# Kernel optimization log

Measured on AMD Instinct MI355X. Metric: run time of the kernel, lower is better.

Reference implementation:

```python
import jax, jax.numpy as jnp
import numpy as np

N_NODE = 2048   # n_node
N_TIME = 10     # t / look_back
STEP_K = 5
PROB_C = 0.98
LN_EPS = 1e-5


def setup_inputs() -> dict:
    key = jax.random.key(0)
    k1, k2 = jax.random.split(key, 2)
    # dynamic adjacency-like input: [n_node, n_time, n_node], nonnegative
    x = jax.random.uniform(k1, (N_NODE, N_TIME, N_NODE), dtype=jnp.float32)
    # learned restart weights, init = prob_c (already in [0,1])
    weight = jnp.full((N_TIME, STEP_K), PROB_C, dtype=jnp.float32)
    # LayerNorm(n_node) params
    ln_gamma = jnp.ones((N_NODE,), dtype=jnp.float32)
    ln_beta = jnp.zeros((N_NODE,), dtype=jnp.float32)
    return {"x": x, "weight": weight, "ln_gamma": ln_gamma, "ln_beta": ln_beta}


def _layer_norm(h, gamma, beta):
    mu = jnp.mean(h, axis=-1, keepdims=True)
    var = jnp.mean((h - mu) ** 2, axis=-1, keepdims=True)
    return (h - mu) * jax.lax.rsqrt(var + LN_EPS) * gamma + beta


def reference(x, weight, ln_gamma, ln_beta):
    # x: [N, T, N]; weight: [T, K]
    w = jnp.clip(weight, 0.0, 1.0)
    n = x.shape[0]
    eye = jnp.eye(n, dtype=x.dtype)  # Pt0

    G = jnp.transpose(x, (1, 0, 2))                 # [T, N, N]
    deg = jnp.sum(G, axis=-1, keepdims=True) + 1e-8  # row degree
    G_norm = G / deg                                # D^{-1} G (row-normalize)

    def per_time(Gt_norm, wt):
        # random walk with restart, accumulate sum of P over K steps
        def step(carry, wi):
            P, acc = carry
            Pc = wi * (P @ Gt_norm) + (1.0 - wi) * eye
            return (Pc, acc + Pc), None
        (_, final_P), _ = jax.lax.scan(step, (eye, jnp.zeros_like(eye)), wt)
        return _layer_norm(final_P, ln_gamma, ln_beta)

    out = jax.vmap(per_time)(G_norm, w)  # [T, N, N]
    return jnp.transpose(out, (1, 0, 2))  # [N, T, N]
```

## Files before the change

kernel.cpp:

```cpp
#include <hip/hip_runtime.h>
#include <stdint.h>

#define NN 2048
#define TT 10
#define KST 5
#define BK 64
#define NKT2 (NN / BK)

typedef float f32x4 __attribute__((ext_vector_type(4)));
typedef __bf16 bf16x8 __attribute__((ext_vector_type(8)));
typedef unsigned short u16x8 __attribute__((ext_vector_type(8)));

using as3_void = __attribute__((address_space(3))) void;
using as1_const_void = const __attribute__((address_space(1))) void;

__device__ __forceinline__ unsigned short f2bf_bits(float f) {
    unsigned u = __builtin_bit_cast(unsigned, f);
    unsigned r = u + 0x7FFFu + ((u >> 16) & 1u);
    return (unsigned short)(r >> 16);
}
__device__ __forceinline__ float bf2f(unsigned short b) {
    return __builtin_bit_cast(float, ((unsigned)b) << 16);
}

__global__ __launch_bounds__(256) void deg_kernel(const float* __restrict__ x,
                                                  float* __restrict__ deg) {
    const int i = blockIdx.x;
    const int t = blockIdx.y;
    const int tid = threadIdx.x;
    const float4* r4 = (const float4*)(x + ((size_t)i * TT + t) * NN);
    float4 a = r4[tid];
    float4 b = r4[tid + 256];
    float s = a.x + a.y + a.z + a.w + b.x + b.y + b.z + b.w;
    #pragma unroll
    for (int m = 32; m >= 1; m >>= 1) s += __shfl_xor(s, m, 64);
    __shared__ float red[4];
    if ((tid & 63) == 0) red[tid >> 6] = s;
    __syncthreads();
    if (tid == 0) deg[(size_t)t * NN + i] = red[0] + red[1] + red[2] + red[3] + 1e-8f;
}

__global__ __launch_bounds__(256) void gnt_init_kernel(const float* __restrict__ x,
                                                       const float* __restrict__ deg,
                                                       const float* __restrict__ w,
                                                       unsigned short* __restrict__ gnt,
                                                       unsigned short* __restrict__ p1,
                                                       int t0) {
    const int tl = blockIdx.z;
    const int t  = t0 + tl;
    float w0 = w[t * KST + 0];
    w0 = fminf(fmaxf(w0, 0.0f), 1.0f);
    const float om = 1.0f - w0;
    const int n0 = blockIdx.x * 64;
    const int k0 = blockIdx.y * 64;
    __shared__ float tile[64][65];
    const int tx = threadIdx.x & 63;
    const int ty = threadIdx.x >> 6;
    unsigned short* p1dst = p1 + (size_t)tl * NN * NN;
    #pragma unroll
    for (int p = 0; p < 16; ++p) {
        int kr = p * 4 + ty;
        float rd = 1.0f / deg[(size_t)t * NN + k0 + kr];
        float v = x[(((size_t)(k0 + kr)) * TT + t) * NN + n0 + tx] * rd;
        tile[kr][tx] = v;
        float pv = w0 * v + ((k0 + kr) == (n0 + tx) ? om : 0.0f);
        p1dst[(size_t)(k0 + kr) * NN + n0 + tx] = f2bf_bits(pv);
    }
    __syncthreads();
    unsigned short* dst = gnt + (size_t)tl * NN * NN;
    #pragma unroll
    for (int p = 0; p < 16; ++p) {
        int nr = p * 4 + ty;
        dst[(size_t)(n0 + nr) * NN + k0 + tx] = f2bf_bits(tile[tx][nr]);
    }
}

#define FENCE __asm__ volatile("" ::: "memory")
#define LGKM0 do { __asm__ volatile("s_waitcnt lgkmcnt(0)" ::: "memory"); \
                   __builtin_amdgcn_sched_barrier(0); } while (0)

#define MFMA_PHASE(PA, PB, BARR)                                                  \
  do {                                                                            \
    _Pragma("unroll")                                                             \
    for (int f_ = 0; f_ < 4; ++f_) {                                              \
      _Pragma("unroll")                                                           \
      for (int g_ = 0; g_ < 2; ++g_) {                                            \
        acc[(PA)*4 + f_][(PB)*2 + g_] = __builtin_amdgcn_mfma_f32_16x16x32_bf16(  \
            af[f_][0], BARR[g_][0], acc[(PA)*4 + f_][(PB)*2 + g_], 0, 0, 0);      \
        acc[(PA)*4 + f_][(PB)*2 + g_] = __builtin_amdgcn_mfma_f32_16x16x32_bf16(  \
            af[f_][1], BARR[g_][1], acc[(PA)*4 + f_][(PB)*2 + g_], 0, 0, 0);      \
      }                                                                           \
    }                                                                             \
  } while (0)

__global__ __launch_bounds__(512, 2) void gemm_step256(
        const unsigned short* __restrict__ Pprev,
        const unsigned short* __restrict__ gnt,
        const float* __restrict__ w,
        unsigned short* __restrict__ Pnext,
        int t0, int kstep) {
    extern __shared__ char smem[];

    const int nwg  = (int)gridDim.x;
    const int flat = (int)blockIdx.x;
    const int xcd  = flat & 7;
    const int q    = nwg >> 3, r = nwg & 7;
    const int wgid = (xcd < r ? xcd * (q + 1) : r * (q + 1) + (xcd - r) * q) + (flat >> 3);
    const int tl   = wgid >> 6;
    const int s    = wgid & 63;
    const int g4   = s >> 2, w4 = s & 3;
    const int tm   = ((g4 >> 2) << 1) | (w4 >> 1);
    const int tn   = ((g4 & 3) << 1) | (w4 & 1);
    const int t    = t0 + tl;

    const int tid  = threadIdx.x;
    const int lane = tid & 63;
    const int wv   = tid >> 6;
    const int wm   = wv >> 2;
    const int wn   = wv & 3;
    const int lr   = lane & 15;
    const int quad = lane >> 4;
    const int swz  = lr & 7;

    const unsigned short* Ab = Pprev + (size_t)tl * NN * NN;
    const unsigned short* Bb = gnt   + (size_t)tl * NN * NN;

    const int srow  = lane >> 3;
    const int sslot = (lane & 7) ^ srow;
    const unsigned short* pa[2][2];
    const unsigned short* pb[2][2];
    #pragma unroll
    for (int h = 0; h < 2; ++h)
        #pragma unroll
        for (int l = 0; l < 2; ++l) {
            const int rA = tm * 256 + h * 128 + l * 64 + wv * 8 + srow;
            const int rB = tn * 256 + h * 128 + l * 64 + wv * 8 + srow;
            pa[h][l] = Ab + (size_t)rA * NN + sslot * 8;
            pb[h][l] = Bb + (size_t)rB * NN + sslot * 8;
        }

    auto stageA = [&](int kt, int b, int h) {
        #pragma unroll
        for (int l = 0; l < 2; ++l)
            __builtin_amdgcn_global_load_lds(
                (as1_const_void*)(pa[h][l] + kt * BK),
                (as3_void*)(smem + b * 65536 + h * 16384 + l * 8192 + wv * 1024),
                16, 0, 0);
    };
    auto stageB = [&](int kt, int b, int h) {
        #pragma unroll
        for (int l = 0; l < 2; ++l)
            __builtin_amdgcn_global_load_lds(
                (as1_const_void*)(pb[h][l] + kt * BK),
                (as3_void*)(smem + b * 65536 + 32768 + h * 16384 + l * 8192 + wv * 1024),
                16, 0, 0);
    };

    bf16x8 af[4][2];
    bf16x8 bf0[2][2];
    bf16x8 bf1[2][2];
    const int sA = ((quad)     ^ swz) * 16;
    const int sB = ((quad + 4) ^ swz) * 16;
    auto lda = [&](int b, int half) {
        const char* base = smem + b * 65536 + half * 16384 + (wm * 64 + lr) * 128;
        #pragma unroll
        for (int f = 0; f < 4; ++f) {
            af[f][0] = *(const bf16x8*)(base + f * 2048 + sA);
            af[f][1] = *(const bf16x8*)(base + f * 2048 + sB);
        }
    };
    auto ldb = [&](int b, int half, bf16x8 (&dst)[2][2]) {
        const char* base = smem + b * 65536 + 32768 + half * 16384 + (wn * 32 + lr) * 128;
        #pragma unroll
        for (int g = 0; g < 2; ++g) {
            dst[g][0] = *(const bf16x8*)(base + g * 2048 + sA);
            dst[g][1] = *(const bf16x8*)(base + g * 2048 + sB);
        }
    };

    f32x4 acc[8][4];
    #pragma unroll
    for (int i = 0; i < 8; ++i)
        #pragma unroll
        for (int j = 0; j < 4; ++j)
            acc[i][j] = (f32x4){0.0f, 0.0f, 0.0f, 0.0f};

    stageA(0, 0, 0);
    stageB(0, 0, 0);
    stageB(0, 0, 1);
    stageA(0, 0, 1);
    stageA(1, 1, 0);
    stageB(1, 1, 0);
    stageB(1, 1, 1);
    FENCE; __builtin_amdgcn_s_waitcnt(0xF76); __builtin_amdgcn_s_barrier(); FENCE;

    for (int kt = 0; kt < NKT2; ++kt) {
        const int b  = kt & 1;
        const int nb = b ^ 1;
        const int k1 = (kt + 1 < NKT2) ? kt + 1 : NKT2 - 1;
        const int k2 = (kt + 2 < NKT2) ? kt + 2 : NKT2 - 1;

        lda(b, 0);
        ldb(b, 0, bf0);
        stageA(k1, nb, 1);
        FENCE; __builtin_amdgcn_s_barrier(); LGKM0;
        __builtin_amdgcn_s_setprio(1);
        MFMA_PHASE(0, 0, bf0);
        __builtin_amdgcn_s_setprio(0);
        FENCE; __builtin_amdgcn_s_barrier(); FENCE;

        ldb(b, 1, bf1);
        stageA(k2, b, 0);
        FENCE; __builtin_amdgcn_s_barrier(); LGKM0;
        __builtin_amdgcn_s_setprio(1);
        MFMA_PHASE(0, 1, bf1);
        __builtin_amdgcn_s_setprio(0);
        FENCE; __builtin_amdgcn_s_barrier(); FENCE;

        lda(b, 1);
        stageB(k2, b, 0);
        FENCE; __builtin_amdgcn_s_barrier(); LGKM0;
        __builtin_amdgcn_s_setprio(1);
        MFMA_PHASE(1, 1, bf1);
        __builtin_amdgcn_s_setprio(0);
        FENCE; __builtin_amdgcn_s_barrier(); FENCE;

        stageB(k2, b, 1);
        __builtin_amdgcn_s_setprio(1);
        MFMA_PHASE(1, 0, bf0);
        __builtin_amdgcn_s_setprio(0);
        FENCE; __builtin_amdgcn_s_waitcnt(0xF76); __builtin_amdgcn_s_barrier(); FENCE;
    }

    float wk = w[t * KST + kstep];
    wk = fminf(fmaxf(wk, 0.0f), 1.0f);
    const float om = 1.0f - wk;
    unsigned short* __restrict__ Pn = Pnext + (size_t)tl * NN * NN;
    #pragma unroll
    for (int F = 0; F < 8; ++F) {
        const int mrow0 = tm * 256 + (F >> 2) * 128 + wm * 64 + (F & 3) * 16 + quad * 4;
        #pragma unroll
        for (int v = 0; v < 4; ++v) {
            const int m = mrow0 + v;
            const size_t mb = (size_t)m * NN;
            #pragma unroll
            for (int G = 0; G < 4; ++G) {
                const int n = tn * 256 + (G >> 1) * 128 + wn * 32 + (G & 1) * 16 + lr;
                float val = wk * acc[F][G][v] + (m == n ? om : 0.0f);
                Pn[mb + n] = f2bf_bits(val);
            }
        }
    }
}

__global__ __launch_bounds__(256) void ln_kernel(const unsigned short* __restrict__ Pall,
                                                 const float* __restrict__ gamma,
                                                 const float* __restrict__ beta,
                                                 float* __restrict__ out,
                                                 int t0, size_t strideK) {
    const int m  = blockIdx.x;
    const int tl = blockIdx.y;
    const int t  = t0 + tl;
    const int tid = threadIdx.x;
    const int j = tid * 8;

    const size_t rbase = (size_t)tl * NN * NN + (size_t)m * NN + j;
    float v[8] = {0, 0, 0, 0, 0, 0, 0, 0};
    #pragma unroll
    for (int k = 0; k < KST; ++k) {
        u16x8 pv = *(const u16x8*)(Pall + (size_t)k * strideK + rbase);
        #pragma unroll
        for (int e = 0; e < 8; ++e) v[e] += bf2f(pv[e]);
    }

    float s = 0.0f;
    #pragma unroll
    for (int e = 0; e < 8; ++e) s += v[e];
    #pragma unroll
    for (int mm = 32; mm >= 1; mm >>= 1) s += __shfl_xor(s, mm, 64);
    __shared__ float red[4];
    if ((tid & 63) == 0) red[tid >> 6] = s;
    __syncthreads();
    const float mu = (red[0] + red[1] + red[2] + red[3]) * (1.0f / NN);

    float q = 0.0f;
    float dx[8];
    #pragma unroll
    for (int e = 0; e < 8; ++e) { dx[e] = v[e] - mu; q += dx[e] * dx[e]; }
    __syncthreads();
    #pragma unroll
    for (int mm = 32; mm >= 1; mm >>= 1) q += __shfl_xor(q, mm, 64);
    if ((tid & 63) == 0) red[tid >> 6] = q;
    __syncthreads();
    const float var = (red[0] + red[1] + red[2] + red[3]) * (1.0f / NN);
    const float sc = rsqrtf(var + 1e-5f);

    float4 g0 = *(const float4*)(gamma + j);
    float4 g1 = *(const float4*)(gamma + j + 4);
    float4 b0 = *(const float4*)(beta + j);
    float4 b1 = *(const float4*)(beta + j + 4);
    const size_t ob = ((size_t)m * TT + t) * NN + j;
    float4 o0, o1;
    o0.x = dx[0] * sc * g0.x + b0.x;  o0.y = dx[1] * sc * g0.y + b0.y;
    o0.z = dx[2] * sc * g0.z + b0.z;  o0.w = dx[3] * sc * g0.w + b0.w;
    o1.x = dx[4] * sc * g1.x + b1.x;  o1.y = dx[5] * sc * g1.y + b1.y;
    o1.z = dx[6] * sc * g1.z + b1.z;  o1.w = dx[7] * sc * g1.w + b1.w;
    *(float4*)(out + ob)     = o0;
    *(float4*)(out + ob + 4) = o1;
}

extern "C" void kernel_launch(void* const* d_in, const int* in_sizes, int n_in,
                              void* d_out, int out_size, void* d_ws, size_t ws_size,
                              hipStream_t stream) {
    (void)in_sizes; (void)n_in; (void)out_size;
    const float* x     = (const float*)d_in[0];
    const float* w     = (const float*)d_in[1];
    const float* gamma = (const float*)d_in[2];
    const float* beta  = (const float*)d_in[3];
    float* out = (float*)d_out;

    static bool attr_done = false;
    if (!attr_done) {
        (void)hipFuncSetAttribute((const void*)gemm_step256,
                                  hipFuncAttributeMaxDynamicSharedMemorySize, 131072);
        attr_done = true;
    }

    char* ws = (char*)d_ws;
    float* deg = (float*)ws;
    size_t off = ((size_t)TT * NN * sizeof(float) + 255) & ~(size_t)255;
    const size_t per_t = (size_t)NN * NN * sizeof(unsigned short);
    size_t avail = ws_size > off ? ws_size - off : 0;
    int TB = (int)(avail / ((1 + KST) * per_t));
    if (TB < 1) TB = 1;
    if (TB > TT) TB = TT;
    unsigned short* gnt  = (unsigned short*)(ws + off);
    unsigned short* Pall = gnt + (size_t)TB * NN * NN;
    const size_t strideK = (size_t)TB * NN * NN;

    deg_kernel<<<dim3(NN, TT), 256, 0, stream>>>(x, deg);

    for (int t0 = 0; t0 < TT; t0 += TB) {
        const int tb = (TT - t0) < TB ? (TT - t0) : TB;
        gnt_init_kernel<<<dim3(32, 32, tb), 256, 0, stream>>>(x, deg, w, gnt, Pall, t0);
        for (int k = 2; k <= KST; ++k) {
            const unsigned short* Pp = Pall + (size_t)(k - 2) * strideK;
            unsigned short*       Pn = Pall + (size_t)(k - 1) * strideK;
            gemm_step256<<<dim3(64 * tb), 512, 131072, stream>>>(Pp, gnt, w, Pn, t0, k - 1);
        }
        ln_kernel<<<dim3(NN, tb), 256, 0, stream>>>(Pall, gamma, beta, out, t0, strideK);
    }
}
```

Before: 1.091 ms.

## Shrink GEMM tile to 128x256 and simplify to a two-phase prefetch pipeline

The GEMM step kernel's workgroup tile goes from 256x256 to 128x256. That halves the A staging, the accumulators and the LDS footprint (96KB instead of 128KB) and doubles the grid to 128 workgroups per time slice, aiming for better load balance and less tail effect. The main loop changes from four MFMA phases with a two-tile-ahead prefetch to two phases with a one-tile-ahead prefetch, synchronised by vmcnt waits and barriers. The cost is lower arithmetic intensity per tile, more global and L2 traffic for the B operand, and a shallower pipeline that may expose memory latency.

```diff
diff --git a/kernel.cpp b/kernel.cpp
--- a/kernel.cpp
+++ b/kernel.cpp
@@ -76,24 +76,22 @@
 }
 
 #define FENCE __asm__ volatile("" ::: "memory")
-#define LGKM0 do { __asm__ volatile("s_waitcnt lgkmcnt(0)" ::: "memory"); \
-                   __builtin_amdgcn_sched_barrier(0); } while (0)
 
 #define MFMA_PHASE(PA, PB, BARR)                                                  \
   do {                                                                            \
     _Pragma("unroll")                                                             \
-    for (int f_ = 0; f_ < 4; ++f_) {                                              \
+    for (int f_ = 0; f_ < 2; ++f_) {                                              \
       _Pragma("unroll")                                                           \
       for (int g_ = 0; g_ < 2; ++g_) {                                            \
-        acc[(PA)*4 + f_][(PB)*2 + g_] = __builtin_amdgcn_mfma_f32_16x16x32_bf16(  \
-            af[f_][0], BARR[g_][0], acc[(PA)*4 + f_][(PB)*2 + g_], 0, 0, 0);      \
-        acc[(PA)*4 + f_][(PB)*2 + g_] = __builtin_amdgcn_mfma_f32_16x16x32_bf16(  \
-            af[f_][1], BARR[g_][1], acc[(PA)*4 + f_][(PB)*2 + g_], 0, 0, 0);      \
+        acc[(PA)*2 + f_][(PB)*2 + g_] = __builtin_amdgcn_mfma_f32_16x16x32_bf16(  \
+            af[f_][0], BARR[g_][0], acc[(PA)*2 + f_][(PB)*2 + g_], 0, 0, 0);      \
+        acc[(PA)*2 + f_][(PB)*2 + g_] = __builtin_amdgcn_mfma_f32_16x16x32_bf16(  \
+            af[f_][1], BARR[g_][1], acc[(PA)*2 + f_][(PB)*2 + g_], 0, 0, 0);      \
       }                                                                           \
     }                                                                             \
   } while (0)
 
-__global__ __launch_bounds__(512, 2) void gemm_step256(
+__global__ __launch_bounds__(512, 2) void gemm_step128(
         const unsigned short* __restrict__ Pprev,
         const unsigned short* __restrict__ gnt,
         const float* __restrict__ w,
@@ -106,12 +104,13 @@
     const int xcd  = flat & 7;
     const int q    = nwg >> 3, r = nwg & 7;
     const int wgid = (xcd < r ? xcd * (q + 1) : r * (q + 1) + (xcd - r) * q) + (flat >> 3);
-    const int tl   = wgid >> 6;
-    const int s    = wgid & 63;
-    const int g4   = s >> 2, w4 = s & 3;
-    const int tm   = ((g4 >> 2) << 1) | (w4 >> 1);
-    const int tn   = ((g4 & 3) << 1) | (w4 & 1);
-    const int t    = t0 + tl;
+    const int tl   = wgid >> 7;
+    const int s    = wgid & 127;
+    const int within = s & 3;
+    const int sup    = s >> 2;
+    const int tm     = (sup >> 2) * 2 + (within >> 1);
+    const int tn     = (sup & 3) * 2 + (within & 1);
+    const int t      = t0 + tl;
 
     const int tid  = threadIdx.x;
     const int lane = tid & 63;
@@ -127,50 +126,49 @@
 
     const int srow  = lane >> 3;
     const int sslot = (lane & 7) ^ srow;
-    const unsigned short* pa[2][2];
+    const unsigned short* pa[2];
     const unsigned short* pb[2][2];
     #pragma unroll
-    for (int h = 0; h < 2; ++h)
+    for (int h = 0; h < 2; ++h) {
+        const int rA = tm * 128 + h * 64 + wv * 8 + srow;
+        pa[h] = Ab + (size_t)rA * NN + sslot * 8;
         #pragma unroll
         for (int l = 0; l < 2; ++l) {
-            const int rA = tm * 256 + h * 128 + l * 64 + wv * 8 + srow;
             const int rB = tn * 256 + h * 128 + l * 64 + wv * 8 + srow;
-            pa[h][l] = Ab + (size_t)rA * NN + sslot * 8;
             pb[h][l] = Bb + (size_t)rB * NN + sslot * 8;
         }
+    }
 
     auto stageA = [&](int kt, int b, int h) {
-        #pragma unroll
-        for (int l = 0; l < 2; ++l)
-            __builtin_amdgcn_global_load_lds(
-                (as1_const_void*)(pa[h][l] + kt * BK),
-                (as3_void*)(smem + b * 65536 + h * 16384 + l * 8192 + wv * 1024),
-                16, 0, 0);
+        __builtin_amdgcn_global_load_lds(
+            (as1_const_void*)(pa[h] + kt * BK),
+            (as3_void*)(smem + b * 49152 + h * 8192 + wv * 1024),
+            16, 0, 0);
     };
     auto stageB = [&](int kt, int b, int h) {
         #pragma unroll
         for (int l = 0; l < 2; ++l)
             __builtin_amdgcn_global_load_lds(
                 (as1_const_void*)(pb[h][l] + kt * BK),
-                (as3_void*)(smem + b * 65536 + 32768 + h * 16384 + l * 8192 + wv * 1024),
+                (as3_void*)(smem + b * 49152 + 16384 + h * 16384 + l * 8192 + wv * 1024),
                 16, 0, 0);
     };
 
-    bf16x8 af[4][2];
+    bf16x8 af[2][2];
     bf16x8 bf0[2][2];
     bf16x8 bf1[2][2];
     const int sA = ((quad)     ^ swz) * 16;
     const int sB = ((quad + 4) ^ swz) * 16;
     auto lda = [&](int b, int half) {
-        const char* base = smem + b * 65536 + half * 16384 + (wm * 64 + lr) * 128;
-        #pragma unroll
-        for (int f = 0; f < 4; ++f) {
+        const char* base = smem + b * 49152 + half * 8192 + (wm * 32 + lr) * 128;
+        #pragma unroll
+        for (int f = 0; f < 2; ++f) {
             af[f][0] = *(const bf16x8*)(base + f * 2048 + sA);
             af[f][1] = *(const bf16x8*)(base + f * 2048 + sB);
         }
     };
     auto ldb = [&](int b, int half, bf16x8 (&dst)[2][2]) {
-        const char* base = smem + b * 65536 + 32768 + half * 16384 + (wn * 32 + lr) * 128;
+        const char* base = smem + b * 49152 + 16384 + half * 16384 + (wn * 32 + lr) * 128;
         #pragma unroll
         for (int g = 0; g < 2; ++g) {
             dst[g][0] = *(const bf16x8*)(base + g * 2048 + sA);
@@ -178,9 +176,9 @@
         }
     };
 
-    f32x4 acc[8][4];
-    #pragma unroll
-    for (int i = 0; i < 8; ++i)
+    f32x4 acc[4][4];
+    #pragma unroll
+    for (int i = 0; i < 4; ++i)
         #pragma unroll
         for (int j = 0; j < 4; ++j)
             acc[i][j] = (f32x4){0.0f, 0.0f, 0.0f, 0.0f};
@@ -189,56 +187,44 @@
     stageB(0, 0, 0);
     stageB(0, 0, 1);
     stageA(0, 0, 1);
-    stageA(1, 1, 0);
-    stageB(1, 1, 0);
-    stageB(1, 1, 1);
-    FENCE; __builtin_amdgcn_s_waitcnt(0xF76); __builtin_amdgcn_s_barrier(); FENCE;
 
     for (int kt = 0; kt < NKT2; ++kt) {
         const int b  = kt & 1;
         const int nb = b ^ 1;
         const int k1 = (kt + 1 < NKT2) ? kt + 1 : NKT2 - 1;
-        const int k2 = (kt + 2 < NKT2) ? kt + 2 : NKT2 - 1;
-
+
+        FENCE; __builtin_amdgcn_s_waitcnt(0xF71); __builtin_amdgcn_s_barrier(); FENCE;
         lda(b, 0);
         ldb(b, 0, bf0);
-        stageA(k1, nb, 1);
-        FENCE; __builtin_amdgcn_s_barrier(); LGKM0;
+        ldb(b, 1, bf1);
+        stageA(k1, nb, 0);
+        stageB(k1, nb, 0);
         __builtin_amdgcn_s_setprio(1);
         MFMA_PHASE(0, 0, bf0);
-        __builtin_amdgcn_s_setprio(0);
-        FENCE; __builtin_amdgcn_s_barrier(); FENCE;
-
-        ldb(b, 1, bf1);
-        stageA(k2, b, 0);
-        FENCE; __builtin_amdgcn_s_barrier(); LGKM0;
-        __builtin_amdgcn_s_setprio(1);
         MFMA_PHASE(0, 1, bf1);
         __builtin_amdgcn_s_setprio(0);
         FENCE; __builtin_amdgcn_s_barrier(); FENCE;
 
+        FENCE; __builtin_amdgcn_s_waitcnt(0xF73); __builtin_amdgcn_s_barrier(); FENCE;
         lda(b, 1);
-        stageB(k2, b, 0);
-        FENCE; __builtin_amdgcn_s_barrier(); LGKM0;
+        stageB(k1, nb, 1);
+        stageA(k1, nb, 1);
         __builtin_amdgcn_s_setprio(1);
         MFMA_PHASE(1, 1, bf1);
+        MFMA_PHASE(1, 0, bf0);
         __builtin_amdgcn_s_setprio(0);
         FENCE; __builtin_amdgcn_s_barrier(); FENCE;
-
-        stageB(k2, b, 1);
-        __builtin_amdgcn_s_setprio(1);
-        MFMA_PHASE(1, 0, bf0);
-        __builtin_amdgcn_s_setprio(0);
-        FENCE; __builtin_amdgcn_s_waitcnt(0xF76); __builtin_amdgcn_s_barrier(); FENCE;
-    }
+    }
+
+    FENCE; __builtin_amdgcn_s_waitcnt(0xF70); FENCE;
 
     float wk = w[t * KST + kstep];
     wk = fminf(fmaxf(wk, 0.0f), 1.0f);
     const float om = 1.0f - wk;
     unsigned short* __restrict__ Pn = Pnext + (size_t)tl * NN * NN;
     #pragma unroll
-    for (int F = 0; F < 8; ++F) {
-        const int mrow0 = tm * 256 + (F >> 2) * 128 + wm * 64 + (F & 3) * 16 + quad * 4;
+    for (int F = 0; F < 4; ++F) {
+        const int mrow0 = tm * 128 + (F >> 1) * 64 + wm * 32 + (F & 1) * 16 + quad * 4;
         #pragma unroll
         for (int v = 0; v < 4; ++v) {
             const int m = mrow0 + v;
@@ -321,8 +307,8 @@
 
     static bool attr_done = false;
     if (!attr_done) {
-        (void)hipFuncSetAttribute((const void*)gemm_step256,
-                                  hipFuncAttributeMaxDynamicSharedMemorySize, 131072);
+        (void)hipFuncSetAttribute((const void*)gemm_step128,
+                                  hipFuncAttributeMaxDynamicSharedMemorySize, 98304);
         attr_done = true;
     }
 
@@ -346,7 +332,7 @@
         for (int k = 2; k <= KST; ++k) {
             const unsigned short* Pp = Pall + (size_t)(k - 2) * strideK;
             unsigned short*       Pn = Pall + (size_t)(k - 1) * strideK;
-            gemm_step256<<<dim3(64 * tb), 512, 131072, stream>>>(Pp, gnt, w, Pn, t0, k - 1);
+            gemm_step128<<<dim3(128 * tb), 512, 98304, stream>>>(Pp, gnt, w, Pn, t0, k - 1);
         }
         ln_kernel<<<dim3(NN, tb), 256, 0, stream>>>(Pall, gamma, beta, out, t0, strideK);
     }
```

Result: slower. 1.263 ms (+15.8%).
